# Kernel optimization log

Hardware: AMD Instinct MI355X
Metric: run time of the kernel (lower is better)

Reference implementation:

```python
import jax, jax.numpy as jnp
import numpy as np

V, C, L, D = 50000, 125000, 500000, 128


def _l2norm(x):
    n = jnp.sqrt(jnp.sum(x * x, axis=-1, keepdims=True))
    return x / jnp.maximum(n, 1e-12)


def _combine(x, W1, b1, W2, b2):
    # SymmetricSumCombine element op: normalize(sigmoid(layer1(x)) + layer2(x));
    # the outer sum over set members is done by segment_sum by the caller.
    return _l2norm(jax.nn.sigmoid(x @ W1 + b1) + (x @ W2 + b2))


def setup_inputs() -> dict:
    key = jax.random.key(0)
    ks = jax.random.split(key, 22)
    s = 1.0 / np.sqrt(D)
    w = lambda k: jax.random.normal(k, (D, D), jnp.float32) * s
    b = lambda k: jax.random.normal(k, (D,), jnp.float32) * s
    return {
        "variables": jax.random.normal(ks[0], (V, D), jnp.float32),
        "lit_var": jax.random.randint(ks[1], (L,), 0, V, jnp.int32),
        "lit_sign": jax.random.randint(ks[2], (L,), 0, 2, jnp.int32),
        "lit_clause": jnp.sort(jax.random.randint(ks[3], (L,), 0, C, jnp.int32)),
        "clause_var": jax.random.randint(ks[4], (C,), 0, V, jnp.int32),
        "neg_W": w(ks[5]), "neg_b": b(ks[6]),
        "vc_W1": w(ks[7]), "vc_b1": b(ks[8]), "vc_W2": w(ks[9]), "vc_b2": b(ks[10]),
        "cc_W1": w(ks[11]), "cc_b1": b(ks[12]), "cc_W2": w(ks[13]), "cc_b2": b(ks[14]),
        "W_z": w(ks[15]), "U_z": w(ks[16]), "W_r": w(ks[17]), "U_r": w(ks[18]),
        "W_h": w(ks[19]), "U_h": w(ks[20]),
    }


def reference(variables, lit_var, lit_sign, lit_clause, clause_var,
              neg_W, neg_b, vc_W1, vc_b1, vc_W2, vc_b2,
              cc_W1, cc_b1, cc_W2, cc_b2,
              W_z, U_z, W_r, U_r, W_h, U_h):
    n_vars = variables.shape[0]
    n_clauses = clause_var.shape[0]
    # gather per-literal variable embeddings, negate negative literals
    v = variables[lit_var]  # [L, D]
    v = jnp.where((lit_sign > 0)[:, None], v @ neg_W + neg_b, v)
    # variable_combiner per literal, summed into clause embeddings
    t = _combine(v, vc_W1, vc_b1, vc_W2, vc_b2)  # [L, D]
    ce = jax.ops.segment_sum(t, lit_clause, num_segments=n_clauses)  # [C, D]
    # clause_combiner per clause, summed into owner variable message
    c = _combine(ce, cc_W1, cc_b1, cc_W2, cc_b2)  # [C, D]
    av = jax.ops.segment_sum(c, clause_var, num_segments=n_vars)  # [V, D]
    # variables with no clauses keep their own embedding as the message
    cnt = jnp.zeros((n_vars,), jnp.float32).at[clause_var].add(1.0)
    av = jnp.where((cnt > 0)[:, None], av, variables)
    # GRU update
    z = jax.nn.sigmoid(av @ W_z + variables @ U_z)
    r = jax.nn.sigmoid(av @ W_r + variables @ U_r)
    h_tilda = jnp.tanh(av @ W_h + (r * variables) @ U_h)
    return (1.0 - z) * variables + z * h_tilda
```

## Files before the change

### kernel.cpp

```cpp
#include <hip/hip_runtime.h>

#define V_N 50000
#define C_N 125000
#define L_N 500000
#define NCH2 31250

typedef __attribute__((ext_vector_type(8))) short short8;
typedef __attribute__((ext_vector_type(4))) float f32x4;

__device__ inline unsigned short f2bf(float f) {
  union { float f; unsigned u; } v; v.f = f;
  unsigned r = v.u + 0x7FFFu + ((v.u >> 16) & 1u);
  return (unsigned short)(r >> 16);
}
__device__ inline float bf2f(unsigned short h) {
  union { unsigned u; float f; } v; v.u = ((unsigned)h) << 16;
  return v.f;
}
__device__ inline float sigm(float x) { return 1.f / (1.f + __expf(-x)); }

struct WPtrs { const float* w[11]; };

__global__ __launch_bounds__(256) void k_front(
    WPtrs p, unsigned short* __restrict__ wt,
    const int* __restrict__ lit_var, const int* __restrict__ lit_sign,
    const int* __restrict__ lit_clause, int* __restrict__ pmeta,
    int* __restrict__ bnd, const int* __restrict__ clause_var,
    int* __restrict__ cnt, int* __restrict__ dst) {
  int b = blockIdx.x;
  if (b < 704) {
    int idx = b * 256 + threadIdx.x;
    int m = idx >> 14;
    int e14 = idx & 16383;
    int chunk = e14 >> 9;
    int rem = e14 & 511;
    int kq = rem >> 7;
    int lan15 = (rem >> 3) & 15;
    int e = rem & 7;
    int col = ((chunk >> 3) << 5) + (((chunk >> 2) & 1) << 4) + lan15;
    int k = ((chunk & 3) << 5) + (kq << 3) + e;
    wt[idx] = f2bf(p.w[m][k * 128 + col]);
  } else if (b < 2658) {
    int i = (b - 704) * 256 + threadIdx.x;
    if (i < L_N)
      pmeta[i] = lit_var[i] | (lit_sign[i] << 16) | ((lit_clause[i] & 63) << 17);
  } else if (b < 2781) {
    int i = (b - 2658) * 256 + threadIdx.x;
    if (i <= NCH2) {
      int key = i * 4;
      int lo = 0, hi = L_N;
      while (lo < hi) {
        int mid = (lo + hi) >> 1;
        if (lit_clause[mid] < key) lo = mid + 1; else hi = mid;
      }
      bnd[i] = lo;
    }
  } else {
    int i = (b - 2781) * 256 + threadIdx.x;
    if (i < C_N) {
      int v = clause_var[i];
      dst[i] = atomicAdd(&cnt[v], 1);
    }
  }
}

__device__ inline void load_bfrags(const unsigned short* __restrict__ Wt,
                                   short8 B[2][4], int wave, int lane) {
#pragma unroll
  for (int ct = 0; ct < 2; ++ct)
#pragma unroll
    for (int ks = 0; ks < 4; ++ks)
      B[ct][ks] = *(const short8*)(Wt + (((wave << 3) + (ct << 2) + ks) << 9) +
                                   (lane << 3));
}

__device__ inline void gemm_reg(const unsigned short (*__restrict__ xs)[136],
                                const short8 B[2][4], f32x4 acc[4][2], int lane) {
  const int lan15 = lane & 15, kq = lane >> 4;
#pragma unroll
  for (int ks = 0; ks < 4; ++ks) {
#pragma unroll
    for (int rt = 0; rt < 4; ++rt) {
      short8 a = *(const short8*)(&xs[rt * 16 + lan15][ks * 32 + kq * 8]);
#pragma unroll
      for (int ct = 0; ct < 2; ++ct)
        acc[rt][ct] = __builtin_amdgcn_mfma_f32_16x16x32_bf16(a, B[ct][ks], acc[rt][ct], 0, 0, 0);
    }
  }
}

__device__ inline void zero_acc(f32x4 acc[4][2]) {
#pragma unroll
  for (int rt = 0; rt < 4; ++rt)
#pragma unroll
    for (int ct = 0; ct < 2; ++ct) acc[rt][ct] = (f32x4)(0.f);
}

__device__ inline void gemm_reg32(const unsigned short (*__restrict__ xs)[136],
                                  const short8 B[2][4], f32x4 acc[2][2], int lane) {
  const int lan15 = lane & 15, kq = lane >> 4;
#pragma unroll
  for (int ks = 0; ks < 4; ++ks) {
#pragma unroll
    for (int rt = 0; rt < 2; ++rt) {
      short8 a = *(const short8*)(&xs[rt * 16 + lan15][ks * 32 + kq * 8]);
#pragma unroll
      for (int ct = 0; ct < 2; ++ct)
        acc[rt][ct] = __builtin_amdgcn_mfma_f32_16x16x32_bf16(a, B[ct][ks], acc[rt][ct], 0, 0, 0);
    }
  }
}

__device__ inline void zero_acc2(f32x4 acc[2][2]) {
#pragma unroll
  for (int rt = 0; rt < 2; ++rt)
#pragma unroll
    for (int ct = 0; ct < 2; ++ct) acc[rt][ct] = (f32x4)(0.f);
}

__device__ inline void stage_f32_32(const float* __restrict__ base, long vb, int nrows,
                                    unsigned short (*__restrict__ dst)[136], int tid) {
  int r = tid >> 3, cq = (tid & 7) * 16;
  long v = vb + r;
  bool valid = v < nrows;
  const float* src = valid ? base + v * 128 : base;
#pragma unroll
  for (int j = 0; j < 16; j += 4) {
    float4 x4 = *(const float4*)(src + cq + j);
    if (!valid) { x4.x = 0.f; x4.y = 0.f; x4.z = 0.f; x4.w = 0.f; }
    dst[r][cq + j + 0] = f2bf(x4.x);
    dst[r][cq + j + 1] = f2bf(x4.y);
    dst[r][cq + j + 2] = f2bf(x4.z);
    dst[r][cq + j + 3] = f2bf(x4.w);
  }
}

__global__ __launch_bounds__(256, 2) void k_tables(
    const float* __restrict__ vars,
    const unsigned short* __restrict__ negWt, const float* __restrict__ negb,
    const unsigned short* __restrict__ W1t, const float* __restrict__ b1,
    const unsigned short* __restrict__ W2t, const float* __restrict__ b2,
    unsigned short* __restrict__ t_pos, unsigned short* __restrict__ t_neg) {
  __shared__ unsigned short xs[32][136];
  __shared__ unsigned short ys[32][136];
  __shared__ float ssp[32][4];
  const int tid = threadIdx.x;
  const int wave = tid >> 6, lane = tid & 63;
  const int lan15 = lane & 15, kq = lane >> 4;
  const long vb = (long)blockIdx.x * 32;

  stage_f32_32(vars, vb, V_N, xs, tid);
  __syncthreads();

  float nb[2], bb1[2], bb2[2];
#pragma unroll
  for (int ct = 0; ct < 2; ++ct) {
    int col = wave * 32 + ct * 16 + lan15;
    nb[ct] = negb[col]; bb1[ct] = b1[col]; bb2[ct] = b2[col];
  }
  {
    short8 BN[2][4];
    load_bfrags(negWt, BN, wave, lane);
    f32x4 acc[2][2];
    zero_acc2(acc);
    gemm_reg32(xs, BN, acc, lane);
#pragma unroll
    for (int rt = 0; rt < 2; ++rt)
#pragma unroll
      for (int ct = 0; ct < 2; ++ct) {
        int col = wave * 32 + ct * 16 + lan15;
#pragma unroll
        for (int reg = 0; reg < 4; ++reg)
          ys[rt * 16 + kq * 4 + reg][col] = f2bf(acc[rt][ct][reg] + nb[ct]);
      }
  }
  __syncthreads();

  short8 B1f[2][4], B2f[2][4];
  load_bfrags(W1t, B1f, wave, lane);
  load_bfrags(W2t, B2f, wave, lane);

#pragma unroll
  for (int pass = 0; pass < 2; ++pass) {
    const unsigned short (*A)[136] = pass ? ys : xs;
    unsigned short* dst = pass ? t_neg : t_pos;
    f32x4 a1[2][2], a2[2][2];
    zero_acc2(a1); zero_acc2(a2);
    gemm_reg32(A, B1f, a1, lane);
    gemm_reg32(A, B2f, a2, lane);
    float s[2][2][4]; float ss[2][4];
#pragma unroll
    for (int rt = 0; rt < 2; ++rt) {
#pragma unroll
      for (int reg = 0; reg < 4; ++reg) ss[rt][reg] = 0.f;
#pragma unroll
      for (int ct = 0; ct < 2; ++ct)
#pragma unroll
        for (int reg = 0; reg < 4; ++reg) {
          float v = sigm(a1[rt][ct][reg] + bb1[ct]) + (a2[rt][ct][reg] + bb2[ct]);
          s[rt][ct][reg] = v; ss[rt][reg] += v * v;
        }
    }
#pragma unroll
    for (int rt = 0; rt < 2; ++rt)
#pragma unroll
      for (int reg = 0; reg < 4; ++reg) {
        float v = ss[rt][reg];
        v += __shfl_xor(v, 1); v += __shfl_xor(v, 2);
        v += __shfl_xor(v, 4); v += __shfl_xor(v, 8);
        if (lan15 == 0) ssp[rt * 16 + kq * 4 + reg][wave] = v;
      }
    __syncthreads();
#pragma unroll
    for (int rt = 0; rt < 2; ++rt)
#pragma unroll
      for (int reg = 0; reg < 4; ++reg) {
        int row = rt * 16 + kq * 4 + reg;
        float tot = ssp[row][0] + ssp[row][1] + ssp[row][2] + ssp[row][3];
        float inv = 1.f / fmaxf(sqrtf(tot), 1e-12f);
        long vr = vb + row;
        if (vr < V_N) {
#pragma unroll
          for (int ct = 0; ct < 2; ++ct)
            dst[vr * 128 + wave * 32 + ct * 16 + lan15] = f2bf(s[rt][ct][reg] * inv);
        }
      }
    __syncthreads();
  }
}

__global__ __launch_bounds__(256) void k_scan_pre(const int* __restrict__ cnt,
                                                  int* __restrict__ bsum) {
  __shared__ int sh[256];
  const int tid = threadIdx.x;
  int i = blockIdx.x * 256 + tid;
  int v = (i < V_N) ? cnt[i] : 0;
  sh[tid] = v;
  __syncthreads();
  for (int off = 1; off < 256; off <<= 1) {
    int add = (tid >= off) ? sh[tid - off] : 0;
    __syncthreads();
    sh[tid] += add;
    __syncthreads();
  }
  if (tid == 255) bsum[blockIdx.x] = sh[255];
}

__global__ __launch_bounds__(256) void k_scan_mid(int* __restrict__ bsum, int nb) {
  __shared__ int sh[256];
  const int tid = threadIdx.x;
  int v = (tid < nb) ? bsum[tid] : 0;
  sh[tid] = v;
  __syncthreads();
  for (int off = 1; off < 256; off <<= 1) {
    int add = (tid >= off) ? sh[tid - off] : 0;
    __syncthreads();
    sh[tid] += add;
    __syncthreads();
  }
  if (tid < nb) bsum[tid] = sh[tid] - v;
}

__global__ __launch_bounds__(256) void k_scan_post(const int* __restrict__ cnt,
                                                   const int* __restrict__ bsum,
                                                   int* __restrict__ col_start) {
  __shared__ int sh[256];
  const int tid = threadIdx.x;
  int i = blockIdx.x * 256 + tid;
  int v = (i < V_N) ? cnt[i] : 0;
  sh[tid] = v;
  __syncthreads();
  for (int off = 1; off < 256; off <<= 1) {
    int add = (tid >= off) ? sh[tid - off] : 0;
    __syncthreads();
    sh[tid] += add;
    __syncthreads();
  }
  if (i < V_N) col_start[i + 1] = sh[tid] + bsum[blockIdx.x];
  if (i == 0) col_start[0] = 0;
}

__global__ __launch_bounds__(256, 4) void k_sc_clause(
    const int* __restrict__ pmeta, const int* __restrict__ bnd,
    const unsigned short* __restrict__ t_pos,
    const unsigned short* __restrict__ t_neg,
    const int* __restrict__ dst, const int* __restrict__ col_start,
    const int* __restrict__ clause_var,
    const unsigned short* __restrict__ W1t, const float* __restrict__ b1,
    const unsigned short* __restrict__ W2t, const float* __restrict__ b2,
    unsigned short* __restrict__ crows) {
  __shared__ unsigned short xs[64][136];
  __shared__ float ssp[64][4];
  __shared__ int dsts[64];
  const int tid = threadIdx.x;
  const int wave = tid >> 6, lane = tid & 63;
  const int lan15 = lane & 15, kq = lane >> 4;
  const int cb = blockIdx.x * 64;

  if (tid < 64) {
    int c = cb + tid;
    dsts[tid] = (c < C_N) ? dst[c] + col_start[clause_var[c]] : -1;
  }

  int bi0 = blockIdx.x * 16 + wave * 4;
  int i0 = bi0 < NCH2 ? bi0 : NCH2;
  int i1 = (bi0 + 4) < NCH2 ? (bi0 + 4) : NCH2;
  int ws = bnd[i0], we = bnd[i1];

  f32x4 acc[8];
#pragma unroll
  for (int s = 0; s < 8; ++s) acc[s] = (f32x4)(0.f);

  const int mtarget = wave * 16 + lan15;

  for (int base = ws; base < we; base += 32) {
    int mm = 0x00FE0000;
    if (lane < 32) {
      int idx = base + lane;
      if (idx < we) mm = pmeta[idx];
    }
    unsigned au[4];
#pragma unroll
    for (int pp = 0; pp < 4; ++pp) {
      int m0 = __shfl(mm, 8 * kq + 2 * pp);
      int m1 = __shfl(mm, 8 * kq + 2 * pp + 1);
      unsigned lo = (((m0 >> 17) & 127) == mtarget) ? 0x3F80u : 0u;
      unsigned hi = (((m1 >> 17) & 127) == mtarget) ? 0x3F800000u : 0u;
      au[pp] = lo | hi;
    }
    unsigned t16[8][8];
#pragma unroll
    for (int e = 0; e < 8; ++e) {
      int mv = __shfl(mm, 8 * kq + e);
      int v = mv & 0xFFFF;
      const unsigned short* rp =
          ((mv & 0x10000) ? t_neg : t_pos) + (long)v * 128 + lan15;
#pragma unroll
      for (int s = 0; s < 8; ++s) t16[e][s] = rp[s * 16];
    }
    union { unsigned u[4]; short8 s8; } ua;
    ua.u[0] = au[0]; ua.u[1] = au[1]; ua.u[2] = au[2]; ua.u[3] = au[3];
#pragma unroll
    for (int s = 0; s < 8; ++s) {
      union { unsigned u[4]; short8 s8; } ub;
#pragma unroll
      for (int d = 0; d < 4; ++d)
        ub.u[d] = t16[2 * d][s] | (t16[2 * d + 1][s] << 16);
      acc[s] = __builtin_amdgcn_mfma_f32_16x16x32_bf16(ua.s8, ub.s8, acc[s], 0, 0, 0);
    }
  }

#pragma unroll
  for (int s = 0; s < 8; ++s)
#pragma unroll
    for (int reg = 0; reg < 4; ++reg)
      xs[wave * 16 + 4 * kq + reg][s * 16 + lan15] = f2bf(acc[s][reg]);
  __syncthreads();

  short8 B1f[2][4], B2f[2][4];
  load_bfrags(W1t, B1f, wave, lane);
  load_bfrags(W2t, B2f, wave, lane);
  float bb1[2], bb2[2];
#pragma unroll
  for (int ct = 0; ct < 2; ++ct) {
    int col = wave * 32 + ct * 16 + lan15;
    bb1[ct] = b1[col]; bb2[ct] = b2[col];
  }
  f32x4 a1[4][2], a2[4][2];
  zero_acc(a1); zero_acc(a2);
  gemm_reg(xs, B1f, a1, lane);
  gemm_reg(xs, B2f, a2, lane);
  float s[4][2][4]; float ss[4][4];
#pragma unroll
  for (int rt = 0; rt < 4; ++rt) {
#pragma unroll
    for (int reg = 0; reg < 4; ++reg) ss[rt][reg] = 0.f;
#pragma unroll
    for (int ct = 0; ct < 2; ++ct)
#pragma unroll
      for (int reg = 0; reg < 4; ++reg) {
        float v = sigm(a1[rt][ct][reg] + bb1[ct]) + (a2[rt][ct][reg] + bb2[ct]);
        s[rt][ct][reg] = v; ss[rt][reg] += v * v;
      }
  }
#pragma unroll
  for (int rt = 0; rt < 4; ++rt)
#pragma unroll
    for (int reg = 0; reg < 4; ++reg) {
      float v = ss[rt][reg];
      v += __shfl_xor(v, 1); v += __shfl_xor(v, 2);
      v += __shfl_xor(v, 4); v += __shfl_xor(v, 8);
      if (lan15 == 0) ssp[rt * 16 + kq * 4 + reg][wave] = v;
    }
  __syncthreads();
#pragma unroll
  for (int rt = 0; rt < 4; ++rt)
#pragma unroll
    for (int reg = 0; reg < 4; ++reg) {
      int row = rt * 16 + kq * 4 + reg;
      float tot = ssp[row][0] + ssp[row][1] + ssp[row][2] + ssp[row][3];
      float inv = 1.f / fmaxf(sqrtf(tot), 1e-12f);
      int dd = dsts[row];
      if (dd >= 0) {
#pragma unroll
        for (int ct = 0; ct < 2; ++ct)
          crows[(long)dd * 128 + wave * 32 + ct * 16 + lan15] =
              f2bf(s[rt][ct][reg] * inv);
      }
    }
}

__global__ __launch_bounds__(256, 2) void k_gru(
    const float* __restrict__ vars,
    const unsigned short* __restrict__ crows, const int* __restrict__ col_start,
    const unsigned short* __restrict__ Wzt, const unsigned short* __restrict__ Uzt,
    const unsigned short* __restrict__ Wrt, const unsigned short* __restrict__ Urt,
    const unsigned short* __restrict__ Wht, const unsigned short* __restrict__ Uht,
    float* __restrict__ out) {
  __shared__ unsigned short as_[32][136];
  __shared__ unsigned short vs[32][136];
  const int tid = threadIdx.x;
  const int wave = tid >> 6, lane = tid & 63;
  const int lan15 = lane & 15, kq = lane >> 4;
  const long vb = (long)blockIdx.x * 32;

  {
    int r = tid >> 3, cq = (tid & 7) * 16;
    long v = vb + r;
    if (v < V_N) {
      int s0 = col_start[v], s1 = col_start[v + 1];
      if (s1 > s0) {
        float acc[16];
#pragma unroll
        for (int j = 0; j < 16; ++j) acc[j] = 0.f;
        for (int t = s0; t < s1; ++t) {
          const unsigned short* rp = crows + (long)t * 128 + cq;
#pragma unroll
          for (int j = 0; j < 16; j += 8) {
            short8 u = *(const short8*)(rp + j);
#pragma unroll
            for (int e = 0; e < 8; ++e) acc[j + e] += bf2f((unsigned short)u[e]);
          }
        }
#pragma unroll
        for (int j = 0; j < 16; ++j) as_[r][cq + j] = f2bf(acc[j]);
      } else {
#pragma unroll
        for (int j = 0; j < 16; j += 4) {
          float4 x4 = *(const float4*)(vars + v * 128 + cq + j);
          as_[r][cq + j + 0] = f2bf(x4.x);
          as_[r][cq + j + 1] = f2bf(x4.y);
          as_[r][cq + j + 2] = f2bf(x4.z);
          as_[r][cq + j + 3] = f2bf(x4.w);
        }
      }
    } else {
#pragma unroll
      for (int j = 0; j < 16; ++j) as_[r][cq + j] = 0;
    }
  }
  stage_f32_32(vars, vb, V_N, vs, tid);
  __syncthreads();

  f32x4 az[2][2];
  zero_acc2(az);
  {
    short8 BA[2][4], BB[2][4];
    load_bfrags(Wzt, BA, wave, lane);
    load_bfrags(Uzt, BB, wave, lane);
    gemm_reg32(as_, BA, az, lane);
    gemm_reg32(vs, BB, az, lane);
  }
  f32x4 ar[2][2];
  zero_acc2(ar);
  {
    short8 BA[2][4], BB[2][4];
    load_bfrags(Wrt, BA, wave, lane);
    load_bfrags(Urt, BB, wave, lane);
    gemm_reg32(as_, BA, ar, lane);
    gemm_reg32(vs, BB, ar, lane);
  }
  __syncthreads();
#pragma unroll
  for (int rt = 0; rt < 2; ++rt)
#pragma unroll
    for (int ct = 0; ct < 2; ++ct) {
      int col = wave * 32 + ct * 16 + lan15;
#pragma unroll
      for (int reg = 0; reg < 4; ++reg) {
        int row = rt * 16 + kq * 4 + reg;
        float rr = sigm(ar[rt][ct][reg]);
        float vf = bf2f(vs[row][col]);
        vs[row][col] = f2bf(rr * vf);
      }
    }
  __syncthreads();
  f32x4 ah[2][2];
  zero_acc2(ah);
  {
    short8 BA[2][4], BB[2][4];
    load_bfrags(Wht, BA, wave, lane);
    load_bfrags(Uht, BB, wave, lane);
    gemm_reg32(as_, BA, ah, lane);
    gemm_reg32(vs, BB, ah, lane);
  }
#pragma unroll
  for (int rt = 0; rt < 2; ++rt)
#pragma unroll
    for (int ct = 0; ct < 2; ++ct) {
      int col = wave * 32 + ct * 16 + lan15;
#pragma unroll
      for (int reg = 0; reg < 4; ++reg) {
        int row = rt * 16 + kq * 4 + reg;
        long v = vb + row;
        if (v < V_N) {
          float z = sigm(az[rt][ct][reg]);
          float h = tanhf(ah[rt][ct][reg]);
          float vf = vars[v * 128 + col];
          out[v * 128 + col] = (1.f - z) * vf + z * h;
        }
      }
    }
}

extern "C" void kernel_launch(void* const* d_in, const int* in_sizes, int n_in,
                              void* d_out, int out_size, void* d_ws, size_t ws_size,
                              hipStream_t stream) {
  const float* vars = (const float*)d_in[0];
  const int* lit_var = (const int*)d_in[1];
  const int* lit_sign = (const int*)d_in[2];
  const int* lit_clause = (const int*)d_in[3];
  const int* clause_var = (const int*)d_in[4];
  const float* negW = (const float*)d_in[5];
  const float* negb = (const float*)d_in[6];
  const float* vcW1 = (const float*)d_in[7];
  const float* vcb1 = (const float*)d_in[8];
  const float* vcW2 = (const float*)d_in[9];
  const float* vcb2 = (const float*)d_in[10];
  const float* ccW1 = (const float*)d_in[11];
  const float* ccb1 = (const float*)d_in[12];
  const float* ccW2 = (const float*)d_in[13];
  const float* ccb2 = (const float*)d_in[14];
  const float* Wz = (const float*)d_in[15];
  const float* Uz = (const float*)d_in[16];
  const float* Wr = (const float*)d_in[17];
  const float* Ur = (const float*)d_in[18];
  const float* Wh = (const float*)d_in[19];
  const float* Uh = (const float*)d_in[20];

  unsigned char* ws = (unsigned char*)d_ws;
  unsigned short* wt = (unsigned short*)ws;
  unsigned short* t_pos = (unsigned short*)(ws + 360448);
  unsigned short* t_neg = (unsigned short*)(ws + 13160448);
  unsigned short* crows = (unsigned short*)(ws + 25960448);
  int* col_start = (int*)(ws + 58000000);
  int* cnt = (int*)(ws + 58300000);
  int* dst = (int*)(ws + 58600000);
  int* bsum = (int*)(ws + 59200000);
  int* bnd = (int*)(ws + 59300000);
  int* pmeta = (int*)(ws + 59500000);
  if (ws_size < (size_t)61500000) return;

  const int NB = (V_N + 255) / 256;

  WPtrs p;
  p.w[0] = negW; p.w[1] = vcW1; p.w[2] = vcW2; p.w[3] = ccW1; p.w[4] = ccW2;
  p.w[5] = Wz; p.w[6] = Uz; p.w[7] = Wr; p.w[8] = Ur; p.w[9] = Wh; p.w[10] = Uh;

  hipMemsetAsync(ws + 58300000, 0, (size_t)200000, stream);
  hipLaunchKernelGGL(k_front, dim3(3270), dim3(256), 0, stream, p, wt,
                     lit_var, lit_sign, lit_clause, pmeta, bnd, clause_var,
                     cnt, dst);

  hipLaunchKernelGGL(k_scan_pre, dim3(NB), dim3(256), 0, stream, cnt, bsum);
  hipLaunchKernelGGL(k_scan_mid, dim3(1), dim3(256), 0, stream, bsum, NB);
  hipLaunchKernelGGL(k_scan_post, dim3(NB), dim3(256), 0, stream, cnt, bsum, col_start);

  hipLaunchKernelGGL(k_tables, dim3((V_N + 31) / 32), dim3(256), 0, stream,
                     vars, wt + 0, negb, wt + 16384, vcb1, wt + 2 * 16384, vcb2,
                     t_pos, t_neg);

  hipLaunchKernelGGL(k_sc_clause, dim3((C_N + 63) / 64), dim3(256), 0, stream,
                     pmeta, bnd, t_pos, t_neg, dst, col_start, clause_var,
                     wt + 3 * 16384, ccb1, wt + 4 * 16384, ccb2, crows);

  hipLaunchKernelGGL(k_gru, dim3((V_N + 31) / 32), dim3(256), 0, stream,
                     vars, crows, col_start,
                     wt + 5 * 16384, wt + 6 * 16384, wt + 7 * 16384,
                     wt + 8 * 16384, wt + 9 * 16384, wt + 10 * 16384,
                     (float*)d_out);
}
```

Baseline: 142.3 us.

## Fold scan middle pass into post kernel, coalesce weight reads, relax clause launch bounds

Removes the single-block k_scan_mid launch by having every k_scan_post block redo the 196-entry block-sum scan in shared memory before applying its prefix. The weight conversion in k_front now reads the fp32 weights contiguously and scatters the bf16 writes into the MFMA-friendly layout, replacing strided gathers. k_sc_clause's launch bounds drop from 4 to 2 waves-per-SIMD hint, allowing more registers at the cost of occupancy. The redundant per-block scan adds a little work to each scan block.

```diff
diff --git a/kernel.cpp b/kernel.cpp
--- a/kernel.cpp
+++ b/kernel.cpp
@@ -31,15 +31,12 @@
   if (b < 704) {
     int idx = b * 256 + threadIdx.x;
     int m = idx >> 14;
-    int e14 = idx & 16383;
-    int chunk = e14 >> 9;
-    int rem = e14 & 511;
-    int kq = rem >> 7;
-    int lan15 = (rem >> 3) & 15;
-    int e = rem & 7;
-    int col = ((chunk >> 3) << 5) + (((chunk >> 2) & 1) << 4) + lan15;
-    int k = ((chunk & 3) << 5) + (kq << 3) + e;
-    wt[idx] = f2bf(p.w[m][k * 128 + col]);
+    int j = idx & 16383;
+    int k = j >> 7, col = j & 127;
+    float val = p.w[m][j];
+    int chunk = ((col >> 5) << 3) + (((col >> 4) & 1) << 2) + (k >> 5);
+    int off = (((k >> 3) & 3) << 7) + ((col & 15) << 3) + (k & 7);
+    wt[m * 16384 + chunk * 512 + off] = f2bf(val);
   } else if (b < 2658) {
     int i = (b - 704) * 256 + threadIdx.x;
     if (i < L_N)
@@ -246,26 +243,23 @@
   if (tid == 255) bsum[blockIdx.x] = sh[255];
 }
 
-__global__ __launch_bounds__(256) void k_scan_mid(int* __restrict__ bsum, int nb) {
-  __shared__ int sh[256];
-  const int tid = threadIdx.x;
-  int v = (tid < nb) ? bsum[tid] : 0;
-  sh[tid] = v;
-  __syncthreads();
-  for (int off = 1; off < 256; off <<= 1) {
-    int add = (tid >= off) ? sh[tid - off] : 0;
-    __syncthreads();
-    sh[tid] += add;
-    __syncthreads();
-  }
-  if (tid < nb) bsum[tid] = sh[tid] - v;
-}
-
 __global__ __launch_bounds__(256) void k_scan_post(const int* __restrict__ cnt,
                                                    const int* __restrict__ bsum,
-                                                   int* __restrict__ col_start) {
+                                                   int* __restrict__ col_start,
+                                                   int nb) {
   __shared__ int sh[256];
+  __shared__ int shb[256];
   const int tid = threadIdx.x;
+  int bv = (tid < nb) ? bsum[tid] : 0;
+  shb[tid] = bv;
+  __syncthreads();
+  for (int off = 1; off < 256; off <<= 1) {
+    int add = (tid >= off) ? shb[tid - off] : 0;
+    __syncthreads();
+    shb[tid] += add;
+    __syncthreads();
+  }
+  int bpref = (blockIdx.x == 0) ? 0 : shb[blockIdx.x - 1];
   int i = blockIdx.x * 256 + tid;
   int v = (i < V_N) ? cnt[i] : 0;
   sh[tid] = v;
@@ -276,11 +270,11 @@
     sh[tid] += add;
     __syncthreads();
   }
-  if (i < V_N) col_start[i + 1] = sh[tid] + bsum[blockIdx.x];
+  if (i < V_N) col_start[i + 1] = sh[tid] + bpref;
   if (i == 0) col_start[0] = 0;
 }
 
-__global__ __launch_bounds__(256, 4) void k_sc_clause(
+__global__ __launch_bounds__(256, 2) void k_sc_clause(
     const int* __restrict__ pmeta, const int* __restrict__ bnd,
     const unsigned short* __restrict__ t_pos,
     const unsigned short* __restrict__ t_neg,
@@ -573,8 +567,8 @@
                      cnt, dst);
 
   hipLaunchKernelGGL(k_scan_pre, dim3(NB), dim3(256), 0, stream, cnt, bsum);
-  hipLaunchKernelGGL(k_scan_mid, dim3(1), dim3(256), 0, stream, bsum, NB);
-  hipLaunchKernelGGL(k_scan_post, dim3(NB), dim3(256), 0, stream, cnt, bsum, col_start);
+  hipLaunchKernelGGL(k_scan_post, dim3(NB), dim3(256), 0, stream, cnt, bsum,
+                     col_start, NB);
 
   hipLaunchKernelGGL(k_tables, dim3((V_N + 31) / 32), dim3(256), 0, stream,
                      vars, wt + 0, negb, wt + 16384, vcb1, wt + 2 * 16384, vcb2,
```

Measured after the change: 146.3 us. 2.8% more time.
